# Kernel tuning notes

Measured on AMD Instinct MI355X. Metric: run time of the kernel, lower is better.

The kernel has to match this reference:

```python
import jax, jax.numpy as jnp
import numpy as np

B, S, D_IN, D_H, D_ACT = 16, 2048, 1024, 2048, 1024


def setup_inputs() -> dict:
    key = jax.random.key(0)
    ks = jax.random.split(key, 8)
    s_in = 1.0 / np.sqrt(D_IN)
    s_h = 1.0 / np.sqrt(D_H)
    return {
        "x": jax.random.normal(ks[0], (B, S, D_IN), dtype=jnp.float32),
        "W_init": jax.random.uniform(ks[1], (D_H, D_IN), jnp.float32, -s_in, s_in),
        "b_init": jax.random.uniform(ks[2], (D_H,), jnp.float32, -s_in, s_in),
        "W_ih": jax.random.uniform(ks[3], (D_H, D_H), jnp.float32, -s_h, s_h),
        "b_ih": jax.random.uniform(ks[4], (D_H,), jnp.float32, -s_h, s_h),
        "b_hh": jax.random.uniform(ks[5], (D_H,), jnp.float32, -s_h, s_h),
        "W_final": jax.random.uniform(ks[6], (D_ACT, D_H), jnp.float32, -s_h, s_h),
        "b_final": jax.random.uniform(ks[7], (D_ACT,), jnp.float32, -s_h, s_h),
    }


def reference(x, W_init, b_init, W_ih, b_ih, b_hh, W_final, b_final):
    # initial linear + relu: [B,S,D_IN] -> [B,S,D_H]
    h = jax.nn.relu(jnp.einsum('bsi,hi->bsh', x, W_init) + b_init)
    # per-timestep RNN with hidden reset to zero each step: the W_hh term
    # vanishes, so each step is relu(W_ih @ h_t + b_ih + b_hh) -> one GEMM.
    out = jax.nn.relu(jnp.einsum('bsh,gh->bsg', h, W_ih) + b_ih + b_hh)
    # final linear: [B,S,D_H] -> [B,S,D_ACT]
    return jnp.einsum('bsh,ah->bsa', out, W_final) + b_final
```

## Files before the change

kernel.cpp:

```cpp
#include <hip/hip_runtime.h>
#include <hip/hip_bf16.h>
#include <stdint.h>
#include <stddef.h>

typedef __bf16 bf16;
typedef __bf16 bf16x8 __attribute__((ext_vector_type(8)));
typedef float f32x4 __attribute__((ext_vector_type(4)));
typedef __attribute__((address_space(1))) void gvoid;
typedef __attribute__((address_space(3))) void lvoid;

#define BM 128
#define BN 128
#define BK 64

__global__ __launch_bounds__(256)
void cvt_f32_bf16(const float* __restrict__ in, bf16* __restrict__ out, int n8)
{
    int i = blockIdx.x * 256 + threadIdx.x;
    if (i >= n8) return;
    const f32x4* p = (const f32x4*)in + (size_t)i * 2;
    f32x4 a = p[0], b = p[1];
    bf16x8 o;
    o[0] = (bf16)a[0]; o[1] = (bf16)a[1]; o[2] = (bf16)a[2]; o[3] = (bf16)a[3];
    o[4] = (bf16)b[0]; o[5] = (bf16)b[1]; o[6] = (bf16)b[2]; o[7] = (bf16)b[3];
    *((bf16x8*)out + i) = o;
}

template<int RELU, int TWO_BIAS, int OUTF32>
__global__ __launch_bounds__(256, 2)
void gemm_bt(const bf16* __restrict__ A, const bf16* __restrict__ Bm,
             const float* __restrict__ bias1, const float* __restrict__ bias2,
             void* __restrict__ Cp, int M, int N, int K)
{
    __shared__ __align__(16) bf16 As[BM * BK];
    __shared__ __align__(16) bf16 Bs[BN * BK];

    const int tid  = threadIdx.x;
    const int wave = tid >> 6;
    const int lane = tid & 63;
    const int bn = blockIdx.x;
    const int bm = blockIdx.y;

    const int wm = (wave >> 1) * 64;
    const int wn = (wave & 1) * 64;

    const int r_in = lane >> 3;
    const int c8   = (((lane & 7) ^ r_in)) * 8;
    const int ch0  = wave * 4;

    const bf16* aG0 = A  + (size_t)(bm * BM + (ch0 + 0) * 8 + r_in) * K + c8;
    const bf16* aG1 = A  + (size_t)(bm * BM + (ch0 + 1) * 8 + r_in) * K + c8;
    const bf16* aG2 = A  + (size_t)(bm * BM + (ch0 + 2) * 8 + r_in) * K + c8;
    const bf16* aG3 = A  + (size_t)(bm * BM + (ch0 + 3) * 8 + r_in) * K + c8;
    const bf16* bG0 = Bm + (size_t)(bn * BN + (ch0 + 0) * 8 + r_in) * K + c8;
    const bf16* bG1 = Bm + (size_t)(bn * BN + (ch0 + 1) * 8 + r_in) * K + c8;
    const bf16* bG2 = Bm + (size_t)(bn * BN + (ch0 + 2) * 8 + r_in) * K + c8;
    const bf16* bG3 = Bm + (size_t)(bn * BN + (ch0 + 3) * 8 + r_in) * K + c8;

    bf16* aL0 = &As[(ch0 + 0) * 512];
    bf16* aL1 = &As[(ch0 + 1) * 512];
    bf16* aL2 = &As[(ch0 + 2) * 512];
    bf16* aL3 = &As[(ch0 + 3) * 512];
    bf16* bL0 = &Bs[(ch0 + 0) * 512];
    bf16* bL1 = &Bs[(ch0 + 1) * 512];
    bf16* bL2 = &Bs[(ch0 + 2) * 512];
    bf16* bL3 = &Bs[(ch0 + 3) * 512];

    const int frow = lane & 15;
    const int g0   = lane >> 4;
    const int fsw  = frow & 7;

    f32x4 acc[4][4];
    #pragma unroll
    for (int i = 0; i < 4; i++)
        #pragma unroll
        for (int j = 0; j < 4; j++)
            acc[i][j] = {0.f, 0.f, 0.f, 0.f};

    for (int k0 = 0; k0 < K; k0 += BK) {
        __builtin_amdgcn_global_load_lds((gvoid*)aG0, (lvoid*)aL0, 16, 0, 0);
        __builtin_amdgcn_global_load_lds((gvoid*)aG1, (lvoid*)aL1, 16, 0, 0);
        __builtin_amdgcn_global_load_lds((gvoid*)aG2, (lvoid*)aL2, 16, 0, 0);
        __builtin_amdgcn_global_load_lds((gvoid*)aG3, (lvoid*)aL3, 16, 0, 0);
        __builtin_amdgcn_global_load_lds((gvoid*)bG0, (lvoid*)bL0, 16, 0, 0);
        __builtin_amdgcn_global_load_lds((gvoid*)bG1, (lvoid*)bL1, 16, 0, 0);
        __builtin_amdgcn_global_load_lds((gvoid*)bG2, (lvoid*)bL2, 16, 0, 0);
        __builtin_amdgcn_global_load_lds((gvoid*)bG3, (lvoid*)bL3, 16, 0, 0);
        aG0 += BK; aG1 += BK; aG2 += BK; aG3 += BK;
        bG0 += BK; bG1 += BK; bG2 += BK; bG3 += BK;
        __syncthreads();

        #pragma unroll
        for (int h = 0; h < 2; h++) {
            const int cg = ((g0 + 4 * h) ^ fsw) * 8;
            bf16x8 af[4], bfr[4];
            #pragma unroll
            for (int i = 0; i < 4; i++)
                af[i] = *(const bf16x8*)&As[(wm + frow + i * 16) * BK + cg];
            #pragma unroll
            for (int j = 0; j < 4; j++)
                bfr[j] = *(const bf16x8*)&Bs[(wn + frow + j * 16) * BK + cg];

            #pragma unroll
            for (int i = 0; i < 4; i++)
                #pragma unroll
                for (int j = 0; j < 4; j++)
                    acc[i][j] = __builtin_amdgcn_mfma_f32_16x16x32_bf16(
                        af[i], bfr[j], acc[i][j], 0, 0, 0);
        }

        __syncthreads();
    }

    const int crow0 = bm * BM + wm + (lane >> 4) * 4;
    const int ccol0 = bn * BN + wn + (lane & 15);

    #pragma unroll
    for (int j = 0; j < 4; j++) {
        const int col = ccol0 + j * 16;
        float bv = bias1[col];
        if (TWO_BIAS) bv += bias2[col];
        #pragma unroll
        for (int i = 0; i < 4; i++) {
            const int row = crow0 + i * 16;
            #pragma unroll
            for (int r = 0; r < 4; r++) {
                float v = acc[i][j][r] + bv;
                if (RELU) v = fmaxf(v, 0.0f);
                if (OUTF32)
                    ((float*)Cp)[(size_t)(row + r) * N + col] = v;
                else
                    ((bf16*)Cp)[(size_t)(row + r) * N + col] = (bf16)v;
            }
        }
    }
}

static inline int cvt_blocks(size_t n) { return (int)((n / 8 + 255) / 256); }

extern "C" void kernel_launch(void* const* d_in, const int* in_sizes, int n_in,
                              void* d_out, int out_size, void* d_ws, size_t ws_size,
                              hipStream_t stream) {
    const float* x       = (const float*)d_in[0];
    const float* W_init  = (const float*)d_in[1];
    const float* b_init  = (const float*)d_in[2];
    const float* W_ih    = (const float*)d_in[3];
    const float* b_ih    = (const float*)d_in[4];
    const float* b_hh    = (const float*)d_in[5];
    const float* W_final = (const float*)d_in[6];
    const float* b_final = (const float*)d_in[7];
    float* out = (float*)d_out;

    const int D_H   = in_sizes[2];
    const int D_IN  = in_sizes[1] / D_H;
    const int D_ACT = in_sizes[7];
    const int M     = in_sizes[0] / D_IN;

    const size_t nx  = (size_t)M * D_IN;
    const size_t nw1 = (size_t)D_H * D_IN;
    const size_t nw2 = (size_t)D_H * D_H;
    const size_t nw3 = (size_t)D_ACT * D_H;
    const size_t nh  = (size_t)M * D_H;

    char* ws  = (char*)d_ws;
    bf16* h   = (bf16*)ws;
    bf16* a2  = (bf16*)(ws + nh * 2);
    bf16* xb  = a2;
    bf16* w1b = (bf16*)(ws + nh * 4);
    bf16* w2b = w1b + nw1;
    bf16* w3b = w2b + nw2;

    cvt_f32_bf16<<<cvt_blocks(nx),  256, 0, stream>>>(x,       xb,  (int)(nx  / 8));
    cvt_f32_bf16<<<cvt_blocks(nw1), 256, 0, stream>>>(W_init,  w1b, (int)(nw1 / 8));
    cvt_f32_bf16<<<cvt_blocks(nw2), 256, 0, stream>>>(W_ih,    w2b, (int)(nw2 / 8));
    cvt_f32_bf16<<<cvt_blocks(nw3), 256, 0, stream>>>(W_final, w3b, (int)(nw3 / 8));

    dim3 blk(256);

    gemm_bt<1, 0, 0><<<dim3(D_H / BN, M / BM), blk, 0, stream>>>(
        xb, w1b, b_init, nullptr, h, M, D_H, D_IN);

    gemm_bt<1, 1, 0><<<dim3(D_H / BN, M / BM), blk, 0, stream>>>(
        h, w2b, b_ih, b_hh, a2, M, D_H, D_H);

    gemm_bt<0, 0, 1><<<dim3(D_ACT / BN, M / BM), blk, 0, stream>>>(
        a2, w3b, b_final, nullptr, out, M, D_ACT, D_H);
}
```

Measured before the change: 792.3 us.

## Rewrite GEMMs as 256x256 tiles with 8 waves and double-buffered LDS pipeline

Replaces the 128x128 single-buffered GEMM with a 256x256 tile kernel using 512 threads, 128KB of dynamic LDS, and double-buffered global-to-LDS staging. Loads for the next K tiles are interleaved between MFMA quadrants, with explicit vmcnt waits, barriers and raised priority around the MFMA blocks. The aim is to hide memory latency and raise arithmetic intensity per tile. In exchange it uses more registers and LDS per block, so occupancy is lower, and the grid is coarser, which risks weaker load balance across CUs.

```diff
diff --git a/kernel.cpp b/kernel.cpp
--- a/kernel.cpp
+++ b/kernel.cpp
@@ -9,9 +9,9 @@
 typedef __attribute__((address_space(1))) void gvoid;
 typedef __attribute__((address_space(3))) void lvoid;
 
-#define BM 128
-#define BN 128
-#define BK 64
+#define FENCE() asm volatile("" ::: "memory")
+#define VMCNT(n) asm volatile("s_waitcnt vmcnt(" #n ")" ::: "memory")
+#define BARS() do { FENCE(); __builtin_amdgcn_s_barrier(); FENCE(); } while (0)
 
 __global__ __launch_bounds__(256)
 void cvt_f32_bf16(const float* __restrict__ in, bf16* __restrict__ out, int n8)
@@ -26,106 +26,148 @@
     *((bf16x8*)out + i) = o;
 }
 
+#define RDA(buf, mh) \
+    _Pragma("unroll") \
+    for (int m_ = 0; m_ < 4; ++m_) { \
+        const int r_ = ((mh) + m_) * 16 + frow; \
+        af[m_][0] = *(const bf16x8*)&As[(buf)*16384 + wr*8192 + r_*64 + ((fg     ^ (r_ & 7)) * 8)]; \
+        af[m_][1] = *(const bf16x8*)&As[(buf)*16384 + wr*8192 + r_*64 + (((fg+4) ^ (r_ & 7)) * 8)]; \
+    }
+
+#define RDB(buf, dst, nb) \
+    _Pragma("unroll") \
+    for (int n_ = 0; n_ < 2; ++n_) { \
+        const int r_ = (wc & 1) * 64 + ((nb) + n_) * 16 + frow; \
+        dst[n_][0] = *(const bf16x8*)&Bs[(buf)*16384 + (wc>>1)*8192 + r_*64 + ((fg     ^ (r_ & 7)) * 8)]; \
+        dst[n_][1] = *(const bf16x8*)&Bs[(buf)*16384 + (wc>>1)*8192 + r_*64 + (((fg+4) ^ (r_ & 7)) * 8)]; \
+    }
+
+#define STAGE(gsrc, lreg, h, kt) do { \
+        const bf16* g_ = (gsrc) + (size_t)((h) * 128) * K + (size_t)(kt) * 64; \
+        bf16* l_ = (lreg) + (h) * 8192 + wave * 1024; \
+        __builtin_amdgcn_global_load_lds((gvoid*)g_,           (lvoid*)l_,         16, 0, 0); \
+        __builtin_amdgcn_global_load_lds((gvoid*)(g_ + rowK8), (lvoid*)(l_ + 512), 16, 0, 0); \
+    } while (0)
+
+#define QUAD(mh, nh, bb) \
+    _Pragma("unroll") \
+    for (int m_ = 0; m_ < 4; ++m_) \
+        _Pragma("unroll") \
+        for (int n_ = 0; n_ < 2; ++n_) { \
+            acc[(mh)+m_][(nh)+n_] = __builtin_amdgcn_mfma_f32_16x16x32_bf16( \
+                af[m_][0], bb[n_][0], acc[(mh)+m_][(nh)+n_], 0, 0, 0); \
+            acc[(mh)+m_][(nh)+n_] = __builtin_amdgcn_mfma_f32_16x16x32_bf16( \
+                af[m_][1], bb[n_][1], acc[(mh)+m_][(nh)+n_], 0, 0, 0); \
+        }
+
 template<int RELU, int TWO_BIAS, int OUTF32>
-__global__ __launch_bounds__(256, 2)
-void gemm_bt(const bf16* __restrict__ A, const bf16* __restrict__ Bm,
+__global__ __launch_bounds__(512, 2)
+void gemm256(const bf16* __restrict__ A, const bf16* __restrict__ Bm,
              const float* __restrict__ bias1, const float* __restrict__ bias2,
              void* __restrict__ Cp, int M, int N, int K)
 {
-    __shared__ __align__(16) bf16 As[BM * BK];
-    __shared__ __align__(16) bf16 Bs[BN * BK];
+    extern __shared__ bf16 smem[];
+    bf16* As = smem;
+    bf16* Bs = smem + 32768;
 
     const int tid  = threadIdx.x;
     const int wave = tid >> 6;
     const int lane = tid & 63;
+    const int wr   = wave >> 2;
+    const int wc   = wave & 3;
     const int bn = blockIdx.x;
     const int bm = blockIdx.y;
 
-    const int wm = (wave >> 1) * 64;
-    const int wn = (wave & 1) * 64;
-
-    const int r_in = lane >> 3;
-    const int c8   = (((lane & 7) ^ r_in)) * 8;
-    const int ch0  = wave * 4;
-
-    const bf16* aG0 = A  + (size_t)(bm * BM + (ch0 + 0) * 8 + r_in) * K + c8;
-    const bf16* aG1 = A  + (size_t)(bm * BM + (ch0 + 1) * 8 + r_in) * K + c8;
-    const bf16* aG2 = A  + (size_t)(bm * BM + (ch0 + 2) * 8 + r_in) * K + c8;
-    const bf16* aG3 = A  + (size_t)(bm * BM + (ch0 + 3) * 8 + r_in) * K + c8;
-    const bf16* bG0 = Bm + (size_t)(bn * BN + (ch0 + 0) * 8 + r_in) * K + c8;
-    const bf16* bG1 = Bm + (size_t)(bn * BN + (ch0 + 1) * 8 + r_in) * K + c8;
-    const bf16* bG2 = Bm + (size_t)(bn * BN + (ch0 + 2) * 8 + r_in) * K + c8;
-    const bf16* bG3 = Bm + (size_t)(bn * BN + (ch0 + 3) * 8 + r_in) * K + c8;
-
-    bf16* aL0 = &As[(ch0 + 0) * 512];
-    bf16* aL1 = &As[(ch0 + 1) * 512];
-    bf16* aL2 = &As[(ch0 + 2) * 512];
-    bf16* aL3 = &As[(ch0 + 3) * 512];
-    bf16* bL0 = &Bs[(ch0 + 0) * 512];
-    bf16* bL1 = &Bs[(ch0 + 1) * 512];
-    bf16* bL2 = &Bs[(ch0 + 2) * 512];
-    bf16* bL3 = &Bs[(ch0 + 3) * 512];
+    const int rc  = lane >> 3;
+    const int sgc = ((lane & 7) ^ rc) * 8;
+    const bf16* aS0 = A  + (size_t)(bm * 256 + wave * 16 + rc) * K + sgc;
+    const bf16* bS0 = Bm + (size_t)(bn * 256 + wave * 16 + rc) * K + sgc;
+    const size_t rowK8 = (size_t)8 * K;
 
     const int frow = lane & 15;
-    const int g0   = lane >> 4;
-    const int fsw  = frow & 7;
-
-    f32x4 acc[4][4];
+    const int fg   = lane >> 4;
+
+    bf16x8 af[4][2], bl[2][2], bh[2][2];
+    f32x4 acc[8][4];
     #pragma unroll
-    for (int i = 0; i < 4; i++)
+    for (int i = 0; i < 8; ++i)
         #pragma unroll
-        for (int j = 0; j < 4; j++)
+        for (int j = 0; j < 4; ++j)
             acc[i][j] = {0.f, 0.f, 0.f, 0.f};
 
-    for (int k0 = 0; k0 < K; k0 += BK) {
-        __builtin_amdgcn_global_load_lds((gvoid*)aG0, (lvoid*)aL0, 16, 0, 0);
-        __builtin_amdgcn_global_load_lds((gvoid*)aG1, (lvoid*)aL1, 16, 0, 0);
-        __builtin_amdgcn_global_load_lds((gvoid*)aG2, (lvoid*)aL2, 16, 0, 0);
-        __builtin_amdgcn_global_load_lds((gvoid*)aG3, (lvoid*)aL3, 16, 0, 0);
-        __builtin_amdgcn_global_load_lds((gvoid*)bG0, (lvoid*)bL0, 16, 0, 0);
-        __builtin_amdgcn_global_load_lds((gvoid*)bG1, (lvoid*)bL1, 16, 0, 0);
-        __builtin_amdgcn_global_load_lds((gvoid*)bG2, (lvoid*)bL2, 16, 0, 0);
-        __builtin_amdgcn_global_load_lds((gvoid*)bG3, (lvoid*)bL3, 16, 0, 0);
-        aG0 += BK; aG1 += BK; aG2 += BK; aG3 += BK;
-        bG0 += BK; bG1 += BK; bG2 += BK; bG3 += BK;
-        __syncthreads();
-
-        #pragma unroll
-        for (int h = 0; h < 2; h++) {
-            const int cg = ((g0 + 4 * h) ^ fsw) * 8;
-            bf16x8 af[4], bfr[4];
-            #pragma unroll
-            for (int i = 0; i < 4; i++)
-                af[i] = *(const bf16x8*)&As[(wm + frow + i * 16) * BK + cg];
-            #pragma unroll
-            for (int j = 0; j < 4; j++)
-                bfr[j] = *(const bf16x8*)&Bs[(wn + frow + j * 16) * BK + cg];
-
-            #pragma unroll
-            for (int i = 0; i < 4; i++)
-                #pragma unroll
-                for (int j = 0; j < 4; j++)
-                    acc[i][j] = __builtin_amdgcn_mfma_f32_16x16x32_bf16(
-                        af[i], bfr[j], acc[i][j], 0, 0, 0);
-        }
-
-        __syncthreads();
-    }
-
-    const int crow0 = bm * BM + wm + (lane >> 4) * 4;
-    const int ccol0 = bn * BN + wn + (lane & 15);
+    const int NT = K >> 6;
+    const int NI = NT >> 1;
+
+    STAGE(bS0, Bs,         0, 0); STAGE(bS0, Bs,         1, 0);
+    STAGE(aS0, As,         0, 0); STAGE(aS0, As,         1, 0);
+    STAGE(bS0, Bs + 16384, 0, 1); STAGE(bS0, Bs + 16384, 1, 1);
+    VMCNT(4);
+    BARS();
+
+    for (int it = 0; it < NI; ++it) {
+        const int t1 = 2 * it + 1;
+        const int t2 = (2 * it + 2 < NT) ? 2 * it + 2 : 0;
+        const int t3 = t2 + 1;
+
+        RDA(0, 0);
+        RDB(0, bl, 0);
+        STAGE(aS0, As + 16384, 0, t1);
+        BARS();
+        __builtin_amdgcn_s_setprio(1); QUAD(0, 0, bl); __builtin_amdgcn_s_setprio(0);
+        BARS();
+        RDB(0, bh, 2);
+        STAGE(aS0, As + 16384, 1, t1);
+        BARS();
+        __builtin_amdgcn_s_setprio(1); QUAD(0, 2, bh); __builtin_amdgcn_s_setprio(0);
+        BARS();
+        RDA(0, 4);
+        STAGE(bS0, Bs, 0, t2);
+        BARS();
+        __builtin_amdgcn_s_setprio(1); QUAD(4, 0, bl); __builtin_amdgcn_s_setprio(0);
+        BARS();
+        STAGE(bS0, Bs, 1, t2);
+        VMCNT(4);
+        BARS();
+        __builtin_amdgcn_s_setprio(1); QUAD(4, 2, bh); __builtin_amdgcn_s_setprio(0);
+        BARS();
+        RDA(1, 0);
+        RDB(1, bl, 0);
+        STAGE(aS0, As, 0, t2);
+        BARS();
+        __builtin_amdgcn_s_setprio(1); QUAD(0, 0, bl); __builtin_amdgcn_s_setprio(0);
+        BARS();
+        RDB(1, bh, 2);
+        STAGE(aS0, As, 1, t2);
+        BARS();
+        __builtin_amdgcn_s_setprio(1); QUAD(0, 2, bh); __builtin_amdgcn_s_setprio(0);
+        BARS();
+        RDA(1, 4);
+        STAGE(bS0, Bs + 16384, 0, t3);
+        BARS();
+        __builtin_amdgcn_s_setprio(1); QUAD(4, 0, bl); __builtin_amdgcn_s_setprio(0);
+        BARS();
+        STAGE(bS0, Bs + 16384, 1, t3);
+        VMCNT(4);
+        BARS();
+        __builtin_amdgcn_s_setprio(1); QUAD(4, 2, bh); __builtin_amdgcn_s_setprio(0);
+        BARS();
+    }
+    VMCNT(0);
+
+    const int crow0 = bm * 256 + wr * 128 + (lane >> 4) * 4;
+    const int ccol0 = bn * 256 + wc * 64 + (lane & 15);
 
     #pragma unroll
-    for (int j = 0; j < 4; j++) {
-        const int col = ccol0 + j * 16;
+    for (int n = 0; n < 4; ++n) {
+        const int col = ccol0 + n * 16;
         float bv = bias1[col];
         if (TWO_BIAS) bv += bias2[col];
         #pragma unroll
-        for (int i = 0; i < 4; i++) {
-            const int row = crow0 + i * 16;
+        for (int m = 0; m < 8; ++m) {
+            const int row = crow0 + m * 16;
             #pragma unroll
-            for (int r = 0; r < 4; r++) {
-                float v = acc[i][j][r] + bv;
+            for (int r = 0; r < 4; ++r) {
+                float v = acc[m][n][r] + bv;
                 if (RELU) v = fmaxf(v, 0.0f);
                 if (OUTF32)
                     ((float*)Cp)[(size_t)(row + r) * N + col] = v;
@@ -170,19 +212,24 @@
     bf16* w2b = w1b + nw1;
     bf16* w3b = w2b + nw2;
 
+    (void)hipFuncSetAttribute(reinterpret_cast<const void*>(&gemm256<1, 0, 0>),
+                              hipFuncAttributeMaxDynamicSharedMemorySize, 131072);
+    (void)hipFuncSetAttribute(reinterpret_cast<const void*>(&gemm256<1, 1, 0>),
+                              hipFuncAttributeMaxDynamicSharedMemorySize, 131072);
+    (void)hipFuncSetAttribute(reinterpret_cast<const void*>(&gemm256<0, 0, 1>),
+                              hipFuncAttributeMaxDynamicSharedMemorySize, 131072);
+
     cvt_f32_bf16<<<cvt_blocks(nx),  256, 0, stream>>>(x,       xb,  (int)(nx  / 8));
     cvt_f32_bf16<<<cvt_blocks(nw1), 256, 0, stream>>>(W_init,  w1b, (int)(nw1 / 8));
     cvt_f32_bf16<<<cvt_blocks(nw2), 256, 0, stream>>>(W_ih,    w2b, (int)(nw2 / 8));
     cvt_f32_bf16<<<cvt_blocks(nw3), 256, 0, stream>>>(W_final, w3b, (int)(nw3 / 8));
 
-    dim3 blk(256);
-
-    gemm_bt<1, 0, 0><<<dim3(D_H / BN, M / BM), blk, 0, stream>>>(
+    gemm256<1, 0, 0><<<dim3(D_H / 256, M / 256), 512, 131072, stream>>>(
         xb, w1b, b_init, nullptr, h, M, D_H, D_IN);
 
-    gemm_bt<1, 1, 0><<<dim3(D_H / BN, M / BM), blk, 0, stream>>>(
+    gemm256<1, 1, 0><<<dim3(D_H / 256, M / 256), 512, 131072, stream>>>(
         h, w2b, b_ih, b_hh, a2, M, D_H, D_H);
 
-    gemm_bt<0, 0, 1><<<dim3(D_ACT / BN, M / BM), blk, 0, stream>>>(
+    gemm256<0, 0, 1><<<dim3(D_ACT / 256, M / 256), 512, 131072, stream>>>(
         a2, w3b, b_final, nullptr, out, M, D_ACT, D_H);
 }
```

Result: no change. 777.9 us (-1.8%).
